# Kernel tuning notes

Measured on AMD Instinct MI355X. Metric: run time of the kernel, lower is better.

## Reference

```python
import jax, jax.numpy as jnp
import numpy as np

N_E = 1024      # codebook_emb_num
E_DIM = 512     # codebook_emb_dim
BETA = 0.25


def setup_inputs() -> dict:
    key = jax.random.key(0)
    k1, k2 = jax.random.split(key)
    z = jax.random.normal(k1, (16, E_DIM, 64, 64), dtype=jnp.float32)
    # nn.Embedding default init: N(0,1)
    codebook = jax.random.normal(k2, (N_E, E_DIM), dtype=jnp.float32)
    return {"z": z, "codebook": codebook}


def reference(z, codebook):
    b, c, h, w = z.shape
    # (B,C,H,W) -> (B,H,W,C) -> (N, e_dim)
    z_p = jnp.transpose(z, (0, 2, 3, 1))
    z_flat = z_p.reshape(-1, c)

    d = (jnp.sum(z_flat * z_flat, axis=1, keepdims=True)
         + jnp.sum(codebook * codebook, axis=1)
         - 2.0 * z_flat @ codebook.T)

    idx = jnp.argmin(d, axis=1)                       # [N]
    # one-hot @ codebook is mathematically a gather
    z_q = codebook[idx].reshape(z_p.shape)            # [B,H,W,C]

    sg = jax.lax.stop_gradient
    e_latent_loss = jnp.mean((sg(z_q) - z_p) ** 2)
    q_latent_loss = jnp.mean((z_q - sg(z_p)) ** 2)
    codebook_loss = q_latent_loss + e_latent_loss * BETA

    # straight-through estimator
    z_q_st = z_p + sg(z_q - z_p)
    z_q_out = jnp.transpose(z_q_st, (0, 3, 1, 2))     # back to (B,C,H,W)
    indices = idx.reshape(b, 1, h, w)
    return z_q_out, codebook_loss, indices
```

## Files before the change

kernel.cpp:

```cpp
#include <hip/hip_runtime.h>

#define N_E   1024
#define E_DIM 512
#define HW_   4096
#define NVEC  65536
#define ZQ_ELEMS 33554432
#define BETA 0.25f
#define DELTA 256.0f

typedef _Float16 half8 __attribute__((ext_vector_type(8), aligned(16)));
typedef float f32x4 __attribute__((ext_vector_type(4)));
typedef unsigned int u32x4 __attribute__((ext_vector_type(4), aligned(16)));

union H16 { _Float16 f; unsigned short u; };
__device__ __forceinline__ unsigned short f2h(float v) { H16 h; h.f = (_Float16)v; return h.u; }

#define GLDS(gp, lp) __builtin_amdgcn_global_load_lds( \
    (const __attribute__((address_space(1))) void*)(gp), \
    (__attribute__((address_space(3))) void*)(lp), 16, 0, 0)

__global__ __launch_bounds__(64) void vq_prep(const float* __restrict__ cb,
    float* __restrict__ ynorm) {
    int j = blockIdx.x, l = threadIdx.x;
    float s = 0.f;
    for (int i = 0; i < 8; ++i) {
        float v = cb[(j << 9) + l + (i << 6)];
        s += v * v;
    }
#pragma unroll
    for (int off = 32; off > 0; off >>= 1) s += __shfl_xor(s, off);
    if (l == 0) ynorm[j] = s * 1024.f;
}

__global__ __launch_bounds__(256) void vq_prepB(const float* __restrict__ cb,
    unsigned short* __restrict__ Bf) {
    int j16 = blockIdx.x;
    int t = threadIdx.x;
#pragma unroll
    for (int s = 0; s < 4; ++s) {
        int G = ((s << 8) + t) << 3;
        int c = G >> 9, w = G & 511;
        int lane = w >> 3;
        int j = (j16 << 4) + (lane & 15);
        int k0 = (c << 5) + ((lane >> 4) << 3);
        const float* p = cb + ((long)j << 9) + k0;
        unsigned short o8[8];
#pragma unroll
        for (int e = 0; e < 8; ++e) {
            H16 hh; hh.f = (_Float16)(32.f * p[e]);
            o8[e] = hh.u;
        }
        *(u32x4*)&Bf[((long)j16 << 13) + G] = *(u32x4*)&o8[0];
    }
}

__global__ __launch_bounds__(256) void vq_pack(const float* __restrict__ z,
    unsigned short* __restrict__ Ah,
    float* __restrict__ zpart, int base_b, int bid0) {
    __shared__ float T[64][65];
    __shared__ float ps[4];
    int bid = blockIdx.x;
    int hw0 = (bid & 63) << 6;
    int c0 = ((bid >> 6) & 7) << 6;
    int bb = (bid >> 9) + base_b;
    int t = threadIdx.x;
    int hl = t & 63, cl = t >> 6;
    const float* zp = z + ((long)((bb << 9) + c0 + cl)) * 4096 + hw0 + hl;
#pragma unroll
    for (int i = 0; i < 16; ++i)
        T[cl + 4 * i][hl] = zp[(long)(4 * i) * 4096];
    __syncthreads();
    int hr = t >> 2, cg = (t & 3) << 4;
    long m = ((long)(bb - base_b) << 12) + hw0 + hr;
    unsigned short h8[16];
    float s = 0.f;
#pragma unroll
    for (int e = 0; e < 16; ++e) {
        float v0 = T[cg + e][hr];
        s += v0 * v0;
        H16 hh; hh.f = (_Float16)(32.f * v0);
        h8[e] = hh.u;
    }
    long o = m * 512 + c0 + cg;
    *(u32x4*)&Ah[o]     = *(u32x4*)&h8[0];
    *(u32x4*)&Ah[o + 8] = *(u32x4*)&h8[8];
#pragma unroll
    for (int off = 32; off > 0; off >>= 1) s += __shfl_xor(s, off);
    if ((t & 63) == 0) ps[t >> 6] = s;
    __syncthreads();
    if (t == 0) zpart[bid0 + bid] = ps[0] + ps[1] + ps[2] + ps[3];
}

#define MERGE2(d1, j1, d2, j2, od1, oj1, od2, oj2) do {                    \
    bool _ow = (od1) < (d1) || ((od1) == (d1) && (oj1) < (j1));            \
    float _nd1 = _ow ? (od1) : (d1); int _nj1 = _ow ? (oj1) : (j1);        \
    float _cd  = _ow ? (d1) : (od1); int _cj  = _ow ? (j1) : (oj1);        \
    float _sd  = _ow ? (od2) : (d2); int _sj  = _ow ? (oj2) : (j2);        \
    bool _cw = _cd < _sd || (_cd == _sd && _cj < _sj);                     \
    (d1) = _nd1; (j1) = _nj1;                                              \
    (d2) = _cw ? _cd : _sd; (j2) = _cw ? _cj : _sj;                        \
} while (0)

__global__ __launch_bounds__(256, 4) void vq_dist(
    const unsigned short* __restrict__ Ah, const unsigned short* __restrict__ Bf,
    const float* __restrict__ ynorm, int* __restrict__ ws_idx,
    float* __restrict__ out_idx, float* __restrict__ bd1g,
    float* __restrict__ bd2g, int* __restrict__ bj2g, int mbase) {

    __shared__ _Float16 sA[2][64][64];
    __shared__ float b1d[256], b2d[256];
    __shared__ int   b1j[256], b2j[256];

    const int t = threadIdx.x;
    const int l = t & 63, wid = t >> 6;
    const int lid = l & 15, kg = l >> 4;
    const int m0 = blockIdx.x << 6;

    const int r8 = l >> 3, sl = l & 7, st = sl ^ r8;
    const unsigned short* gpA0 = Ah + ((long)(m0 + (wid << 3) + r8) << 9)
                                    + ((st & 4) << 3) + ((st & 3) << 3);

    auto STAGE = [&](int buf, int cpair) {
        const long ao = (long)cpair << 6;
#pragma unroll
        for (int g = 0; g < 2; ++g)
            GLDS(gpA0 + ao + ((long)g << 14), &sA[buf][(wid + (g << 2)) << 3][0]);
    };

    f32x4 acc[4][4];
    auto ZERO = [&]() {
#pragma unroll
        for (int mt = 0; mt < 4; ++mt)
#pragma unroll
            for (int jt = 0; jt < 4; ++jt) acc[mt][jt] = {0.f, 0.f, 0.f, 0.f};
    };

    auto COMPUTE = [&](int buf, int sub, int c, int p) {
        half8 ah[4];
        const int q0 = sub << 2;
#pragma unroll
        for (int mt = 0; mt < 4; ++mt) {
            int row = (mt << 4) + lid;
            ah[mt] = *(const half8*)&sA[buf][row][((q0 + kg) ^ (row & 7)) << 3];
        }
        long fb = (((long)(((p << 4) + (wid << 2)) << 4) + c) << 9) + (l << 3);
        const unsigned short* bp = Bf + fb;
#pragma unroll
        for (int jt = 0; jt < 4; ++jt) {
            half8 bh = *(const half8*)(bp);
            bp += 8192;
#pragma unroll
            for (int mt = 0; mt < 4; ++mt)
                acc[mt][jt] = __builtin_amdgcn_mfma_f32_16x16x32_f16(ah[mt], bh, acc[mt][jt], 0, 0, 0);
        }
    };

    auto FOLD = [&](int p) {
        const int jgb = (p << 8) + (wid << 6);
        float yn[4];
#pragma unroll
        for (int jt = 0; jt < 4; ++jt) yn[jt] = ynorm[jgb + (jt << 4) + lid];
#pragma unroll
        for (int mt = 0; mt < 4; ++mt)
#pragma unroll
            for (int r = 0; r < 4; ++r) {
                float d1 = 3.4e38f, d2 = 3.4e38f;
                int   i1 = 0x7fffffff, i2 = 0x7fffffff;
#pragma unroll
                for (int jt = 0; jt < 4; ++jt) {
                    int jg = jgb + (jt << 4) + lid;
                    float d = yn[jt] - 2.f * acc[mt][jt][r];
                    bool w = d < d1 || (d == d1 && jg < i1);
                    if (w) { d2 = d1; i2 = i1; d1 = d; i1 = jg; }
                    else if (d < d2 || (d == d2 && jg < i2)) { d2 = d; i2 = jg; }
                }
#pragma unroll
                for (int off = 1; off < 16; off <<= 1) {
                    float od1 = __shfl_xor(d1, off), od2 = __shfl_xor(d2, off);
                    int   oi1 = __shfl_xor(i1, off), oi2 = __shfl_xor(i2, off);
                    MERGE2(d1, i1, d2, i2, od1, oi1, od2, oi2);
                }
                if (lid == 0) {
                    int slot = (((mt << 4) + (kg << 2) + r) << 2) + wid;
                    float D1 = b1d[slot], D2 = b2d[slot];
                    int   J1 = b1j[slot], J2 = b2j[slot];
                    MERGE2(D1, J1, D2, J2, d1, i1, d2, i2);
                    b1d[slot] = D1; b1j[slot] = J1;
                    b2d[slot] = D2; b2j[slot] = J2;
                }
            }
    };

    b1d[t] = 3.4e38f; b2d[t] = 3.4e38f;
    b1j[t] = 0x7fffffff; b2j[t] = 0x7fffffff;
    ZERO();
    STAGE(0, 0);
    __syncthreads();

    int buf = 0;
    for (int cp = 0; cp < 32; ++cp) {
        int p = cp >> 3, pc = cp & 7;
        if (cp < 31) STAGE(buf ^ 1, (cp + 1) & 7);
        COMPUTE(buf, 0, (pc << 1),     p);
        COMPUTE(buf, 1, (pc << 1) + 1, p);
        if (pc == 7) { FOLD(p); ZERO(); }
        __syncthreads();
        buf ^= 1;
    }

    if (t < 64) {
        float D1 = 3.4e38f, D2 = 3.4e38f;
        int   J1 = 0x7fffffff, J2 = 0x7fffffff;
#pragma unroll
        for (int w = 0; w < 4; ++w) {
            int slot = (t << 2) + w;
            MERGE2(D1, J1, D2, J2, b1d[slot], b1j[slot], b2d[slot], b2j[slot]);
        }
        int m = mbase + m0 + t;
        ws_idx[m]  = J1;
        out_idx[m] = (float)J1;
        bd1g[m] = D1;
        bd2g[m] = D2;
        bj2g[m] = J2;
    }
}

__global__ __launch_bounds__(256) void vq_refine(const float* __restrict__ z,
    const float* __restrict__ cb, const float* __restrict__ ynorm,
    const float* __restrict__ bd2, const int* __restrict__ bj2,
    int* __restrict__ ws_idx, float* __restrict__ out_idx, float* __restrict__ bd1) {
    int l = threadIdx.x & 63;
    int wv = (blockIdx.x << 2) + (threadIdx.x >> 6);
    for (int m = wv; m < NVEC; m += 4096) {
        float d1 = bd1[m];
        if (bd2[m] - d1 > DELTA) continue;
        int j1 = ws_idx[m], j2 = bj2[m];
        const float* zr = z + ((long)(m >> 12) << 21) + (m & 4095);
        const float* c1 = cb + ((long)j1 << 9);
        const float* c2 = cb + ((long)j2 << 9);
        float s1 = 0.f, s2 = 0.f;
#pragma unroll
        for (int e = 0; e < 8; ++e) {
            int c = (l << 3) + e;
            float a = zr[(long)c << 12];
            s1 = fmaf(a, c1[c], s1);
            s2 = fmaf(a, c2[c], s2);
        }
#pragma unroll
        for (int off = 32; off > 0; off >>= 1) {
            s1 += __shfl_xor(s1, off);
            s2 += __shfl_xor(s2, off);
        }
        float de1 = ynorm[j1] - 2048.f * s1;
        float de2 = ynorm[j2] - 2048.f * s2;
        bool take2 = de2 < de1 || (de2 == de1 && j2 < j1);
        if (l == 0) {
            if (take2) { ws_idx[m] = j2; out_idx[m] = (float)j2; bd1[m] = de2; }
            else       { bd1[m] = de1; }
        }
    }
}

__global__ __launch_bounds__(256) void vq_gather(const float* __restrict__ cb,
    const int* __restrict__ ws_idx, float* __restrict__ out) {
    int base = blockIdx.x * 256 + threadIdx.x;
    int hw  = base & 4095;
    int c4g = (base >> 12) & 31;
    int b   = base >> 17;
    int j   = ws_idx[(b << 12) | hw];
#pragma unroll
    for (int it = 0; it < 4; ++it) {
        int c4 = (c4g << 2) + it;
        float4 v = ((const float4*)cb)[(j << 7) + c4];
        long zo = ((long)((b << 9) + (c4 << 2))) * 4096 + hw;
        out[zo] = v.x; out[zo + 4096] = v.y; out[zo + 8192] = v.z; out[zo + 12288] = v.w;
    }
}

__global__ __launch_bounds__(1024) void vq_final(const float* __restrict__ bd1,
    const float* __restrict__ zpart, float* __restrict__ out) {
    int t = threadIdx.x;
    double s = 0.0;
#pragma unroll
    for (int i = 0; i < 64; ++i) s += (double)bd1[t + (i << 10)];
    s *= (1.0 / 1024.0);
#pragma unroll
    for (int i = 0; i < 8; ++i) s += (double)zpart[t + (i << 10)];
#pragma unroll
    for (int off = 32; off > 0; off >>= 1) s += __shfl_xor(s, off);
    __shared__ double pd[16];
    if ((t & 63) == 0) pd[t >> 6] = s;
    __syncthreads();
    if (t == 0) {
        double tot = 0.0;
#pragma unroll
        for (int i = 0; i < 16; ++i) tot += pd[i];
        out[ZQ_ELEMS] = (float)(1.25 * tot / 33554432.0);
    }
}

extern "C" void kernel_launch(void* const* d_in, const int* in_sizes, int n_in,
                              void* d_out, int out_size, void* d_ws, size_t ws_size,
                              hipStream_t stream) {
    const float* z  = (const float*)d_in[0];
    const float* cb = (const float*)d_in[1];
    float* out = (float*)d_out;
    char* ws = (char*)d_ws;

    float* ynorm = (float*)(ws + 1024);
    int*   ws_idx = (int*)(ws + 8192);
    float* bd1   = (float*)(ws + 272 * 1024);
    float* bd2   = (float*)(ws + 528 * 1024);
    int*   bj2   = (int*)(ws + 784 * 1024);
    float* zpart = (float*)(ws + 1040 * 1024);
    unsigned short* Bf = (unsigned short*)(ws + (2L << 20));
    const size_t base = 4L << 20;
    unsigned short* Ah = (unsigned short*)(ws + base);

    int nphase = 1;
    while (nphase < 16) {
        size_t Asz = (size_t)(65536 / nphase) * 512 * 2;
        if (base + Asz <= ws_size) break;
        nphase <<= 1;
    }

    vq_prep<<<N_E, 64, 0, stream>>>(cb, ynorm);
    vq_prepB<<<64, 256, 0, stream>>>(cb, Bf);
    int PM = 65536 / nphase;
    for (int p = 0; p < nphase; ++p) {
        vq_pack<<<8192 / nphase, 256, 0, stream>>>(z, Ah, zpart,
                                                   p * (16 / nphase),
                                                   p * (8192 / nphase));
        vq_dist<<<PM / 64, 256, 0, stream>>>(Ah, Bf, ynorm, ws_idx,
                                             out + ZQ_ELEMS + 1, bd1, bd2, bj2, p * PM);
    }
    vq_refine<<<1024, 256, 0, stream>>>(z, cb, ynorm, bd2, bj2, ws_idx,
                                        out + ZQ_ELEMS + 1, bd1);
    vq_gather<<<NVEC / 256 * 32, 256, 0, stream>>>(cb, ws_idx, out);
    vq_final<<<1, 1024, 0, stream>>>(bd1, zpart, out);
}
```

Before: 225.5 us.

## Fuse z transpose/fp16 packing into distance kernel with full-K LDS tile

Removes the separate pack kernel and its global fp16 staging buffer. Each 512-thread block now loads a 128-row z tile straight from NCHW, converts it to fp16 into a 128KB swizzled LDS tile covering the whole K, computes ||z||^2 partials, and runs all four codebook passes against that tile. Tie-breaking in the top-2 merge is simplified to branchless selects. This saves a full write and read of the packed activations, but the 128KB LDS allocation limits occupancy to one block per CU, leaving only 512 blocks for the grid.

```diff
diff --git a/kernel.cpp b/kernel.cpp
--- a/kernel.cpp
+++ b/kernel.cpp
@@ -13,11 +13,6 @@
 typedef unsigned int u32x4 __attribute__((ext_vector_type(4), aligned(16)));
 
 union H16 { _Float16 f; unsigned short u; };
-__device__ __forceinline__ unsigned short f2h(float v) { H16 h; h.f = (_Float16)v; return h.u; }
-
-#define GLDS(gp, lp) __builtin_amdgcn_global_load_lds( \
-    (const __attribute__((address_space(1))) void*)(gp), \
-    (__attribute__((address_space(3))) void*)(lp), 16, 0, 0)
 
 __global__ __launch_bounds__(64) void vq_prep(const float* __restrict__ cb,
     float* __restrict__ ynorm) {
@@ -54,78 +49,27 @@
     }
 }
 
-__global__ __launch_bounds__(256) void vq_pack(const float* __restrict__ z,
-    unsigned short* __restrict__ Ah,
-    float* __restrict__ zpart, int base_b, int bid0) {
-    __shared__ float T[64][65];
-    __shared__ float ps[4];
-    int bid = blockIdx.x;
-    int hw0 = (bid & 63) << 6;
-    int c0 = ((bid >> 6) & 7) << 6;
-    int bb = (bid >> 9) + base_b;
-    int t = threadIdx.x;
-    int hl = t & 63, cl = t >> 6;
-    const float* zp = z + ((long)((bb << 9) + c0 + cl)) * 4096 + hw0 + hl;
-#pragma unroll
-    for (int i = 0; i < 16; ++i)
-        T[cl + 4 * i][hl] = zp[(long)(4 * i) * 4096];
-    __syncthreads();
-    int hr = t >> 2, cg = (t & 3) << 4;
-    long m = ((long)(bb - base_b) << 12) + hw0 + hr;
-    unsigned short h8[16];
-    float s = 0.f;
-#pragma unroll
-    for (int e = 0; e < 16; ++e) {
-        float v0 = T[cg + e][hr];
-        s += v0 * v0;
-        H16 hh; hh.f = (_Float16)(32.f * v0);
-        h8[e] = hh.u;
-    }
-    long o = m * 512 + c0 + cg;
-    *(u32x4*)&Ah[o]     = *(u32x4*)&h8[0];
-    *(u32x4*)&Ah[o + 8] = *(u32x4*)&h8[8];
-#pragma unroll
-    for (int off = 32; off > 0; off >>= 1) s += __shfl_xor(s, off);
-    if ((t & 63) == 0) ps[t >> 6] = s;
-    __syncthreads();
-    if (t == 0) zpart[bid0 + bid] = ps[0] + ps[1] + ps[2] + ps[3];
-}
-
-#define MERGE2(d1, j1, d2, j2, od1, oj1, od2, oj2) do {                    \
-    bool _ow = (od1) < (d1) || ((od1) == (d1) && (oj1) < (j1));            \
-    float _nd1 = _ow ? (od1) : (d1); int _nj1 = _ow ? (oj1) : (j1);        \
-    float _cd  = _ow ? (d1) : (od1); int _cj  = _ow ? (j1) : (oj1);        \
-    float _sd  = _ow ? (od2) : (d2); int _sj  = _ow ? (oj2) : (j2);        \
-    bool _cw = _cd < _sd || (_cd == _sd && _cj < _sj);                     \
-    (d1) = _nd1; (j1) = _nj1;                                              \
-    (d2) = _cw ? _cd : _sd; (j2) = _cw ? _cj : _sj;                        \
-} while (0)
-
-__global__ __launch_bounds__(256, 4) void vq_dist(
-    const unsigned short* __restrict__ Ah, const unsigned short* __restrict__ Bf,
+__global__ __launch_bounds__(512, 2) void vq_fused(
+    const float* __restrict__ z, const unsigned short* __restrict__ Bf,
     const float* __restrict__ ynorm, int* __restrict__ ws_idx,
     float* __restrict__ out_idx, float* __restrict__ bd1g,
-    float* __restrict__ bd2g, int* __restrict__ bj2g, int mbase) {
-
-    __shared__ _Float16 sA[2][64][64];
-    __shared__ float b1d[256], b2d[256];
-    __shared__ int   b1j[256], b2j[256];
+    float* __restrict__ bd2g, int* __restrict__ bj2g,
+    float* __restrict__ zpart) {
+
+    __shared__ _Float16 sA[128][512];
+    __shared__ float b1d[128][4], b2d[128][4];
+    __shared__ int   b1j[128][4], b2j[128][4];
+    __shared__ float psum[8];
 
     const int t = threadIdx.x;
     const int l = t & 63, wid = t >> 6;
     const int lid = l & 15, kg = l >> 4;
-    const int m0 = blockIdx.x << 6;
-
-    const int r8 = l >> 3, sl = l & 7, st = sl ^ r8;
-    const unsigned short* gpA0 = Ah + ((long)(m0 + (wid << 3) + r8) << 9)
-                                    + ((st & 4) << 3) + ((st & 3) << 3);
-
-    auto STAGE = [&](int buf, int cpair) {
-        const long ao = (long)cpair << 6;
-#pragma unroll
-        for (int g = 0; g < 2; ++g)
-            GLDS(gpA0 + ao + ((long)g << 14), &sA[buf][(wid + (g << 2)) << 3][0]);
-    };
+    const int wm = (wid >> 2) << 6;
+    const int jw = wid & 3;
+    const int m0 = blockIdx.x << 7;
+
+    b1d[wm + l][jw] = 3.4e38f; b2d[wm + l][jw] = 3.4e38f;
+    b1j[wm + l][jw] = 0x7fffffff; b2j[wm + l][jw] = 0x7fffffff;
 
     f32x4 acc[4][4];
     auto ZERO = [&]() {
@@ -135,19 +79,18 @@
             for (int jt = 0; jt < 4; ++jt) acc[mt][jt] = {0.f, 0.f, 0.f, 0.f};
     };
 
-    auto COMPUTE = [&](int buf, int sub, int c, int p) {
+    auto COMPUTE = [&](int c, int p) {
         half8 ah[4];
-        const int q0 = sub << 2;
 #pragma unroll
         for (int mt = 0; mt < 4; ++mt) {
-            int row = (mt << 4) + lid;
-            ah[mt] = *(const half8*)&sA[buf][row][((q0 + kg) ^ (row & 7)) << 3];
-        }
-        long fb = (((long)(((p << 4) + (wid << 2)) << 4) + c) << 9) + (l << 3);
-        const unsigned short* bp = Bf + fb;
+            int row = wm + (mt << 4) + lid;
+            ah[mt] = *(const half8*)&sA[row][(((c << 2) + kg) ^ (row & 7)) << 3];
+        }
+        const unsigned short* bp = Bf + ((long)((p << 4) + (jw << 2)) << 13)
+                                      + ((long)c << 9) + (l << 3);
 #pragma unroll
         for (int jt = 0; jt < 4; ++jt) {
-            half8 bh = *(const half8*)(bp);
+            half8 bh = *(const half8*)bp;
             bp += 8192;
 #pragma unroll
             for (int mt = 0; mt < 4; ++mt)
@@ -156,7 +99,7 @@
     };
 
     auto FOLD = [&](int p) {
-        const int jgb = (p << 8) + (wid << 6);
+        const int jgb = (p << 8) + (jw << 6);
         float yn[4];
 #pragma unroll
         for (int jt = 0; jt < 4; ++jt) yn[jt] = ynorm[jgb + (jt << 4) + lid];
@@ -165,63 +108,110 @@
 #pragma unroll
             for (int r = 0; r < 4; ++r) {
                 float d1 = 3.4e38f, d2 = 3.4e38f;
-                int   i1 = 0x7fffffff, i2 = 0x7fffffff;
+                int i1 = 0x7fffffff, i2 = 0x7fffffff;
 #pragma unroll
                 for (int jt = 0; jt < 4; ++jt) {
                     int jg = jgb + (jt << 4) + lid;
                     float d = yn[jt] - 2.f * acc[mt][jt][r];
-                    bool w = d < d1 || (d == d1 && jg < i1);
-                    if (w) { d2 = d1; i2 = i1; d1 = d; i1 = jg; }
-                    else if (d < d2 || (d == d2 && jg < i2)) { d2 = d; i2 = jg; }
+                    bool w = d < d1;
+                    float c2 = w ? d1 : d;  int c2i = w ? i1 : jg;
+                    d1 = w ? d : d1;        i1 = w ? jg : i1;
+                    bool u = c2 < d2;
+                    d2 = u ? c2 : d2;       i2 = u ? c2i : i2;
                 }
 #pragma unroll
                 for (int off = 1; off < 16; off <<= 1) {
-                    float od1 = __shfl_xor(d1, off), od2 = __shfl_xor(d2, off);
-                    int   oi1 = __shfl_xor(i1, off), oi2 = __shfl_xor(i2, off);
-                    MERGE2(d1, i1, d2, i2, od1, oi1, od2, oi2);
+                    float e1 = __shfl_xor(d1, off), e2 = __shfl_xor(d2, off);
+                    int   k1 = __shfl_xor(i1, off), k2 = __shfl_xor(i2, off);
+                    bool w = e1 < d1;
+                    float mx = w ? d1 : e1;  int nx = w ? i1 : k1;
+                    d1 = w ? e1 : d1;        i1 = w ? k1 : i1;
+                    bool a = e2 < d2;  float mm = a ? e2 : d2;  int nm = a ? k2 : i2;
+                    bool bb = mx < mm;
+                    d2 = bb ? mx : mm;  i2 = bb ? nx : nm;
                 }
                 if (lid == 0) {
-                    int slot = (((mt << 4) + (kg << 2) + r) << 2) + wid;
-                    float D1 = b1d[slot], D2 = b2d[slot];
-                    int   J1 = b1j[slot], J2 = b2j[slot];
-                    MERGE2(D1, J1, D2, J2, d1, i1, d2, i2);
-                    b1d[slot] = D1; b1j[slot] = J1;
-                    b2d[slot] = D2; b2j[slot] = J2;
+                    int row = wm + (mt << 4) + (kg << 2) + r;
+                    float D1 = b1d[row][jw], D2 = b2d[row][jw];
+                    int   J1 = b1j[row][jw], J2 = b2j[row][jw];
+                    bool w = d1 < D1;
+                    float mx = w ? D1 : d1;  int nx = w ? J1 : i1;
+                    float N1 = w ? d1 : D1;  int NJ1 = w ? i1 : J1;
+                    bool a = d2 < D2;  float mm = a ? d2 : D2;  int nm = a ? i2 : J2;
+                    bool bb = mx < mm;
+                    b1d[row][jw] = N1;            b1j[row][jw] = NJ1;
+                    b2d[row][jw] = bb ? mx : mm;  b2j[row][jw] = bb ? nx : nm;
                 }
             }
     };
 
-    b1d[t] = 3.4e38f; b2d[t] = 3.4e38f;
-    b1j[t] = 0x7fffffff; b2j[t] = 0x7fffffff;
+    float zs = 0.f;
+    const float* zb = z + ((long)(m0 >> 12) << 21) + (m0 & 4095);
+    const int hwq = (t & 31) << 2;
+    const int cl  = t >> 5;
+
     ZERO();
-    STAGE(0, 0);
+    float4 r0 = *(const float4*)&zb[((long)cl << 12) + hwq];
+    float4 r1 = *(const float4*)&zb[((long)(cl + 16) << 12) + hwq];
+    float4 n0 = {0, 0, 0, 0}, n1 = {0, 0, 0, 0};
+
+    for (int c = 0; c < 16; ++c) {
+        if (c < 15) {
+            int cn = ((c + 1) << 5) + cl;
+            n0 = *(const float4*)&zb[((long)cn << 12) + hwq];
+            n1 = *(const float4*)&zb[((long)(cn + 16) << 12) + hwq];
+        }
+        const float* p0 = (const float*)&r0;
+        const float* p1 = (const float*)&r1;
+        int c0 = (c << 5) + cl, c1 = c0 + 16;
+#pragma unroll
+        for (int e = 0; e < 4; ++e) {
+            int row = hwq + e;
+            float v0 = p0[e], v1 = p1[e];
+            zs += v0 * v0 + v1 * v1;
+            sA[row][(((c0 >> 3) ^ (row & 7)) << 3) + (c0 & 7)] = (_Float16)(32.f * v0);
+            sA[row][(((c1 >> 3) ^ (row & 7)) << 3) + (c1 & 7)] = (_Float16)(32.f * v1);
+        }
+        __syncthreads();
+        COMPUTE(c, 0);
+        r0 = n0; r1 = n1;
+    }
+    FOLD(0); ZERO();
+
+    for (int p = 1; p < 4; ++p) {
+        for (int c = 0; c < 16; ++c) COMPUTE(c, p);
+        FOLD(p); ZERO();
+    }
+
+#pragma unroll
+    for (int off = 32; off > 0; off >>= 1) zs += __shfl_xor(zs, off);
+    if (l == 0) psum[wid] = zs;
     __syncthreads();
 
-    int buf = 0;
-    for (int cp = 0; cp < 32; ++cp) {
-        int p = cp >> 3, pc = cp & 7;
-        if (cp < 31) STAGE(buf ^ 1, (cp + 1) & 7);
-        COMPUTE(buf, 0, (pc << 1),     p);
-        COMPUTE(buf, 1, (pc << 1) + 1, p);
-        if (pc == 7) { FOLD(p); ZERO(); }
-        __syncthreads();
-        buf ^= 1;
-    }
-
-    if (t < 64) {
-        float D1 = 3.4e38f, D2 = 3.4e38f;
-        int   J1 = 0x7fffffff, J2 = 0x7fffffff;
-#pragma unroll
-        for (int w = 0; w < 4; ++w) {
-            int slot = (t << 2) + w;
-            MERGE2(D1, J1, D2, J2, b1d[slot], b1j[slot], b2d[slot], b2j[slot]);
-        }
-        int m = mbase + m0 + t;
+    if (t < 128) {
+        float D1 = b1d[t][0], D2 = b2d[t][0];
+        int   J1 = b1j[t][0], J2 = b2j[t][0];
+#pragma unroll
+        for (int w2 = 1; w2 < 4; ++w2) {
+            float e1 = b1d[t][w2], e2 = b2d[t][w2];
+            int   k1 = b1j[t][w2], k2 = b2j[t][w2];
+            bool w = e1 < D1;
+            float mx = w ? D1 : e1;  int nx = w ? J1 : k1;
+            D1 = w ? e1 : D1;        J1 = w ? k1 : J1;
+            bool a = e2 < D2;  float mm = a ? e2 : D2;  int nm = a ? k2 : J2;
+            bool bb = mx < mm;
+            D2 = bb ? mx : mm;  J2 = bb ? nx : nm;
+        }
+        int m = m0 + t;
         ws_idx[m]  = J1;
         out_idx[m] = (float)J1;
-        bd1g[m] = D1;
-        bd2g[m] = D2;
-        bj2g[m] = J2;
+        bd1g[m] = D1; bd2g[m] = D2; bj2g[m] = J2;
+    }
+    if (t == 0) {
+        float tot = 0.f;
+#pragma unroll
+        for (int i = 0; i < 8; ++i) tot += psum[i];
+        zpart[blockIdx.x] = tot;
     }
 }
 
@@ -284,8 +274,7 @@
 #pragma unroll
     for (int i = 0; i < 64; ++i) s += (double)bd1[t + (i << 10)];
     s *= (1.0 / 1024.0);
-#pragma unroll
-    for (int i = 0; i < 8; ++i) s += (double)zpart[t + (i << 10)];
+    if (t < 512) s += (double)zpart[t];
 #pragma unroll
     for (int off = 32; off > 0; off >>= 1) s += __shfl_xor(s, off);
     __shared__ double pd[16];
@@ -314,26 +303,11 @@
     int*   bj2   = (int*)(ws + 784 * 1024);
     float* zpart = (float*)(ws + 1040 * 1024);
     unsigned short* Bf = (unsigned short*)(ws + (2L << 20));
-    const size_t base = 4L << 20;
-    unsigned short* Ah = (unsigned short*)(ws + base);
-
-    int nphase = 1;
-    while (nphase < 16) {
-        size_t Asz = (size_t)(65536 / nphase) * 512 * 2;
-        if (base + Asz <= ws_size) break;
-        nphase <<= 1;
-    }
 
     vq_prep<<<N_E, 64, 0, stream>>>(cb, ynorm);
     vq_prepB<<<64, 256, 0, stream>>>(cb, Bf);
-    int PM = 65536 / nphase;
-    for (int p = 0; p < nphase; ++p) {
-        vq_pack<<<8192 / nphase, 256, 0, stream>>>(z, Ah, zpart,
-                                                   p * (16 / nphase),
-                                                   p * (8192 / nphase));
-        vq_dist<<<PM / 64, 256, 0, stream>>>(Ah, Bf, ynorm, ws_idx,
-                                             out + ZQ_ELEMS + 1, bd1, bd2, bj2, p * PM);
-    }
+    vq_fused<<<512, 512, 0, stream>>>(z, Bf, ynorm, ws_idx,
+                                      out + ZQ_ELEMS + 1, bd1, bd2, bj2, zpart);
     vq_refine<<<1024, 256, 0, stream>>>(z, cb, ynorm, bd2, bj2, ws_idx,
                                         out + ZQ_ELEMS + 1, bd1);
     vq_gather<<<NVEC / 256 * 32, 256, 0, stream>>>(cb, ws_idx, out);
```

Measured after the change: 351.2 us. +55.8%, slower.
